# Performance work log

Measured on AMD Instinct MI355X. Metric: run time of the kernel, lower is better.

Reference implementation:

```python
import jax, jax.numpy as jnp
import numpy as np

NUM_CLUSTERS = 8
NUM_ITERS = 3
SIM_TEMP = 10.0
EPS = 1e-12  # F.normalize default eps


def _l2norm(x):
    n = jnp.linalg.norm(x, axis=-1, keepdims=True)
    return x / jnp.maximum(n, EPS)


def setup_inputs() -> dict:
    key = jax.random.key(0)
    ks = jax.random.split(key, 5)
    B, P, C = 8, 16384, 256
    F_p = jax.random.normal(ks[0], (B, P, C), dtype=jnp.float32)
    scale = 1.0 / np.sqrt(C)
    proj_w = jax.random.normal(ks[1], (C, C), dtype=jnp.float32) * scale
    proj_b = jax.random.normal(ks[2], (C,), dtype=jnp.float32) * scale
    refine_w = jax.random.normal(ks[3], (C, C), dtype=jnp.float32) * scale
    refine_b = jax.random.normal(ks[4], (C,), dtype=jnp.float32) * scale
    return {"F_p": F_p, "proj_w": proj_w, "proj_b": proj_b,
            "refine_w": refine_w, "refine_b": refine_b}


def reference(F_p, proj_w, proj_b, refine_w, refine_b):
    B, P, C = F_p.shape
    c = min(NUM_CLUSTERS, P)
    nodes = F_p @ proj_w.T + proj_b  # (B, P, C)
    # initial centers: evenly spaced node indices (torch.linspace(...).long())
    idx = jnp.asarray(np.linspace(0, P - 1, c).astype(np.int64))
    centers = nodes[:, idx, :]  # (B, c, C)
    nodes_norm = _l2norm(nodes)
    for _ in range(NUM_ITERS):
        sim = jnp.einsum('bpc,bkc->bpk', nodes_norm, _l2norm(centers))
        assignments = jnp.argmax(sim, axis=-1)  # (B, P)
        onehot = jax.nn.one_hot(assignments, c, dtype=nodes.dtype)  # (B, P, c)
        counts = jnp.maximum(onehot.sum(axis=1), 1.0)  # (B, c), clamp(min=1)
        # masked mean per cluster == segment mean via one-hot contraction
        centers = jnp.einsum('bpk,bpc->bkc', onehot, nodes) / counts[..., None]
    sim = jnp.einsum('bpc,bkc->bpk', nodes_norm, _l2norm(centers))
    weights = jax.nn.softmax(sim * SIM_TEMP, axis=-1)  # (B, P, c)
    clustered = jnp.einsum('bpk,bkc->bpc', weights, centers)
    return (clustered + F_p) @ refine_w.T + refine_b
```

## Files before the change

kernel.cpp:

```cpp
#include <hip/hip_runtime.h>
#include <hip/hip_bf16.h>
#include <cmath>

#define BB 8
#define PP 16384
#define CC 256
#define NCLUS 8
#define BPROWS (BB*PP)

typedef unsigned int uint;
typedef unsigned short ushort;
typedef __bf16 bf16x8 __attribute__((ext_vector_type(8)));
typedef float f32x16 __attribute__((ext_vector_type(16)));

__device__ __forceinline__ float bflo(uint u){ return __uint_as_float(u << 16); }
__device__ __forceinline__ float bfhi(uint u){ return __uint_as_float(u & 0xffff0000u); }
__device__ __forceinline__ ushort f2bf(float x){ __hip_bfloat16 h = __float2bfloat16(x); return *(ushort*)&h; }
__device__ __forceinline__ uint pk2(float a, float b){ return (uint)f2bf(a) | ((uint)f2bf(b) << 16); }

__global__ __launch_bounds__(256) void wcvt(const float* __restrict__ Wp,
    const float* __restrict__ Wr, ushort* __restrict__ Wpb, ushort* __restrict__ Wrb) {
  int i = blockIdx.x*256 + threadIdx.x;
  float4 a = *(const float4*)(Wp + (size_t)i*4);
  float4 b = *(const float4*)(Wr + (size_t)i*4);
  *(uint2*)(Wpb + (size_t)i*4) = make_uint2(pk2(a.x,a.y), pk2(a.z,a.w));
  *(uint2*)(Wrb + (size_t)i*4) = make_uint2(pk2(b.x,b.y), pk2(b.z,b.w));
}

__global__ __launch_bounds__(256) void fcvt(const float* __restrict__ F, ushort* __restrict__ fb) {
  size_t i = ((size_t)blockIdx.x*256 + threadIdx.x) * 16;
  float4 a = *(const float4*)(F + i);
  float4 b = *(const float4*)(F + i + 4);
  float4 c = *(const float4*)(F + i + 8);
  float4 d = *(const float4*)(F + i + 12);
  *(uint4*)(fb + i)     = make_uint4(pk2(a.x,a.y), pk2(a.z,a.w), pk2(b.x,b.y), pk2(b.z,b.w));
  *(uint4*)(fb + i + 8) = make_uint4(pk2(c.x,c.y), pk2(c.z,c.w), pk2(d.x,d.y), pk2(d.z,d.w));
}

template<bool PROJ>
__global__ __launch_bounds__(512) void gemm_bf16(const ushort* __restrict__ Ab,
    const ushort* __restrict__ Wb, const float* __restrict__ bias,
    void* __restrict__ Dv, float* __restrict__ rnorm,
    const float* __restrict__ W8, const float* __restrict__ CR) {
  __shared__ __align__(16) char AlB[128*64*2];
  __shared__ __align__(16) char WlB[256*64*2];
  __shared__ float rnp[128][4];
  const int t  = threadIdx.x;
  const int p0 = blockIdx.x * 128;
  const int lane = t & 63;
  const int w  = t >> 6;
  const int wr = w >> 2, wc = w & 3;

  const ushort* asrc[2]; char* adst[2];
  #pragma unroll
  for (int i = 0; i < 2; ++i) {
    int S = i*512 + t, row = S >> 3, sc = S & 7;
    asrc[i] = Ab + (size_t)(p0 + row)*CC + ((sc ^ (row & 7)) << 3);
    adst[i] = AlB + (size_t)S*16;
  }
  const ushort* wsrc[4]; char* wdst[4];
  #pragma unroll
  for (int i = 0; i < 4; ++i) {
    int S = i*512 + t, row = S >> 3, sc = S & 7;
    wsrc[i] = Wb + (size_t)row*CC + ((sc ^ (row & 7)) << 3);
    wdst[i] = WlB + (size_t)S*16;
  }
  const int arow = (wr << 6) + (lane & 31);
  const int brow = (wc << 6) + (lane & 31);
  const int kb0  = (lane >> 5) << 4;

  f32x16 acc[2][2];
  #pragma unroll
  for (int fm = 0; fm < 2; ++fm)
    #pragma unroll
    for (int fn = 0; fn < 2; ++fn)
      #pragma unroll
      for (int r = 0; r < 16; ++r) acc[fm][fn][r] = 0.0f;

  #pragma unroll
  for (int ks = 0; ks < 4; ++ks) {
    #pragma unroll
    for (int i = 0; i < 2; ++i)
      __builtin_amdgcn_global_load_lds(
          (const __attribute__((address_space(1))) uint*)(asrc[i] + ks*64),
          (__attribute__((address_space(3))) uint*)adst[i], 16, 0, 0);
    #pragma unroll
    for (int i = 0; i < 4; ++i)
      __builtin_amdgcn_global_load_lds(
          (const __attribute__((address_space(1))) uint*)(wsrc[i] + ks*64),
          (__attribute__((address_space(3))) uint*)wdst[i], 16, 0, 0);
    __syncthreads();
    bf16x8 af[2][4], bg[2][4];
    #pragma unroll
    for (int fm = 0; fm < 2; ++fm)
      #pragma unroll
      for (int kq = 0; kq < 4; ++kq) {
        int row = arow + (fm << 5);
        int off = row*128 + (((kq << 5) + kb0) ^ ((row & 7) << 4));
        af[fm][kq] = *(const bf16x8*)(AlB + off);
      }
    #pragma unroll
    for (int fn = 0; fn < 2; ++fn)
      #pragma unroll
      for (int kq = 0; kq < 4; ++kq) {
        int row = brow + (fn << 5);
        int off = row*128 + (((kq << 5) + kb0) ^ ((row & 7) << 4));
        bg[fn][kq] = *(const bf16x8*)(WlB + off);
      }
    #pragma unroll
    for (int kq = 0; kq < 4; ++kq)
      #pragma unroll
      for (int fm = 0; fm < 2; ++fm)
        #pragma unroll
        for (int fn = 0; fn < 2; ++fn)
          acc[fm][fn] = __builtin_amdgcn_mfma_f32_32x32x16_bf16(
              af[fm][kq], bg[fn][kq], acc[fm][fn], 0, 0, 0);
    if (ks < 3) __syncthreads();
  }

  const int colb = (wc << 6) + (lane & 31);
  const float b0 = bias[colb], b1 = bias[colb + 32];
  float cr0[8], cr1[8];
  if constexpr (!PROJ) {
    const float* crb = CR + (size_t)(blockIdx.x >> 7)*NCLUS*CC;
    #pragma unroll
    for (int k = 0; k < 8; ++k) { cr0[k] = crb[k*CC + colb]; cr1[k] = crb[k*CC + colb + 32]; }
  }
  #pragma unroll
  for (int fm = 0; fm < 2; ++fm) {
    float rs[16];
    #pragma unroll
    for (int r = 0; r < 16; ++r) {
      int rowin = (r & 3) + ((r >> 2) << 3) + ((lane >> 5) << 2);
      size_t grow = (size_t)(p0 + (wr << 6) + (fm << 5) + rowin);
      float v0 = acc[fm][0][r] + b0;
      float v1 = acc[fm][1][r] + b1;
      if constexpr (PROJ) {
        ushort* D = (ushort*)Dv;
        D[grow*CC + colb]      = f2bf(v0);
        D[grow*CC + colb + 32] = f2bf(v1);
        rs[r] = v0*v0 + v1*v1;
      } else {
        float4 ua = *(const float4*)(W8 + grow*8);
        float4 ub = *(const float4*)(W8 + grow*8 + 4);
        v0 += ua.x*cr0[0] + ua.y*cr0[1] + ua.z*cr0[2] + ua.w*cr0[3]
            + ub.x*cr0[4] + ub.y*cr0[5] + ub.z*cr0[6] + ub.w*cr0[7];
        v1 += ua.x*cr1[0] + ua.y*cr1[1] + ua.z*cr1[2] + ua.w*cr1[3]
            + ub.x*cr1[4] + ub.y*cr1[5] + ub.z*cr1[6] + ub.w*cr1[7];
        float* D = (float*)Dv;
        D[grow*CC + colb]      = v0;
        D[grow*CC + colb + 32] = v1;
      }
    }
    if constexpr (PROJ) {
      #pragma unroll
      for (int m = 1; m < 32; m <<= 1)
        #pragma unroll
        for (int r = 0; r < 16; ++r) rs[r] += __shfl_xor(rs[r], m);
      if ((lane & 31) == 0) {
        #pragma unroll
        for (int r = 0; r < 16; ++r) {
          int rowin = (r & 3) + ((r >> 2) << 3) + ((lane >> 5) << 2);
          rnp[(wr << 6) + (fm << 5) + rowin][wc] = rs[r];
        }
      }
    }
  }
  if constexpr (PROJ) {
    __syncthreads();
    if (t < 128) {
      float s = rnp[t][0] + rnp[t][1] + rnp[t][2] + rnp[t][3];
      rnorm[p0 + t] = 1.0f / fmaxf(sqrtf(s), 1e-12f);
    }
  }
}

__global__ void init_centers(const ushort* __restrict__ nbf, float* __restrict__ centers) {
  const int idx[8] = {0, 2340, 4680, 7021, 9361, 11702, 14042, 16383};
  int b = blockIdx.x >> 3, k = blockIdx.x & 7;
  int c = threadIdx.x;
  centers[(size_t)(b*NCLUS + k)*CC + c] =
      __uint_as_float(((uint)nbf[((size_t)b*PP + idx[k])*CC + c]) << 16);
}

__global__ __launch_bounds__(256) void center_norm_init(const float* __restrict__ centers,
    ushort* __restrict__ cnormbf, float* __restrict__ accs, float* __restrict__ counts) {
  const int row = blockIdx.x;
  const int t = threadIdx.x;
  float c = centers[(size_t)row*CC + t];
  float s2 = c*c;
  #pragma unroll
  for (int o = 32; o; o >>= 1) s2 += __shfl_xor(s2, o);
  __shared__ float ps[4];
  if ((t & 63) == 0) ps[t >> 6] = s2;
  __syncthreads();
  float tot = ps[0] + ps[1] + ps[2] + ps[3];
  cnormbf[(size_t)row*CC + t] = f2bf(c * (1.0f / fmaxf(sqrtf(tot), 1e-12f)));
  #pragma unroll
  for (int s = 0; s < 8; ++s) accs[((size_t)s*64 + row)*CC + t] = 0.0f;
  if (t == 0) counts[row] = 0.0f;
}

__global__ __launch_bounds__(256) void centers_finalize(float* __restrict__ accs,
    float* __restrict__ counts, ushort* __restrict__ cnormbf, float* __restrict__ centers) {
  const int row = blockIdx.x;
  const int t = threadIdx.x;
  float v = 0.0f;
  #pragma unroll
  for (int s = 0; s < 8; ++s) {
    v += accs[((size_t)s*64 + row)*CC + t];
    accs[((size_t)s*64 + row)*CC + t] = 0.0f;
  }
  float cnt = fmaxf(counts[row], 1.0f);
  float c = v / cnt;
  centers[(size_t)row*CC + t] = c;
  float s2 = c*c;
  #pragma unroll
  for (int o = 32; o; o >>= 1) s2 += __shfl_xor(s2, o);
  __shared__ float ps[4];
  if ((t & 63) == 0) ps[t >> 6] = s2;
  __syncthreads();
  float tot = ps[0] + ps[1] + ps[2] + ps[3];
  cnormbf[(size_t)row*CC + t] = f2bf(c * (1.0f / fmaxf(sqrtf(tot), 1e-12f)));
  if (t == 0) counts[row] = 0.0f;
}

__global__ __launch_bounds__(256) void cr8_compute(const float* __restrict__ centers,
    const float* __restrict__ Wr, float* __restrict__ CR) {
  __shared__ float cenL[NCLUS][CC];
  const int b = blockIdx.x;
  const int t = threadIdx.x;
  for (int i = t; i < NCLUS*CC; i += 256)
    ((float*)cenL)[i] = centers[(size_t)b*NCLUS*CC + i];
  __syncthreads();
  float a8[8] = {0,0,0,0,0,0,0,0};
  const float* wrow = Wr + (size_t)t*CC;
  for (int j = 0; j < CC; j += 4) {
    float4 wv = *(const float4*)(wrow + j);
    #pragma unroll
    for (int k = 0; k < 8; ++k) {
      float4 cv = *(const float4*)&cenL[k][j];
      a8[k] += cv.x*wv.x + cv.y*wv.y + cv.z*wv.z + cv.w*wv.w;
    }
  }
  #pragma unroll
  for (int k = 0; k < 8; ++k) CR[((size_t)b*NCLUS + k)*CC + t] = a8[k];
}

__device__ __forceinline__ void sims_mfma(const ushort* __restrict__ nb_base,
    const ushort* __restrict__ cnb, int lane, float* s) {
  const int pcol = lane & 31;
  const int kb   = (lane >> 5) << 3;
  const ushort* arow = cnb + (size_t)(pcol & 7)*CC + kb;
  const ushort* brow = nb_base + (size_t)pcol*CC + kb;
  const bool azero = pcol >= 8;
  bf16x8 z;
  #pragma unroll
  for (int j = 0; j < 8; ++j) z[j] = (__bf16)0.0f;
  f32x16 acc;
  #pragma unroll
  for (int r = 0; r < 16; ++r) acc[r] = 0.0f;
  #pragma unroll
  for (int st = 0; st < 16; ++st) {
    bf16x8 af = *(const bf16x8*)(arow + st*16);
    if (azero) af = z;
    bf16x8 bg = *(const bf16x8*)(brow + st*16);
    acc = __builtin_amdgcn_mfma_f32_32x32x16_bf16(af, bg, acc, 0, 0, 0);
  }
  float sh[4];
  #pragma unroll
  for (int r = 0; r < 4; ++r) sh[r] = __shfl_xor(acc[r], 32);
  const bool hi = lane >= 32;
  #pragma unroll
  for (int r = 0; r < 4; ++r) {
    s[r]     = hi ? sh[r]  : acc[r];
    s[r + 4] = hi ? acc[r] : sh[r];
  }
}

__global__ __launch_bounds__(256) void assign_mfma(const ushort* __restrict__ nbf,
    const ushort* __restrict__ cnormbf, float* __restrict__ accs, float* __restrict__ counts) {
  __shared__ int assignL[128];
  __shared__ int cntL[NCLUS];
  const int t = threadIdx.x;
  const int wave = t >> 6, lane = t & 63;
  const int b = blockIdx.x >> 7;
  if (t < NCLUS) cntL[t] = 0;
  __syncthreads();
  const size_t p0w = (size_t)blockIdx.x*128 + wave*32;
  float s[8];
  sims_mfma(nbf + p0w*CC, cnormbf + (size_t)b*NCLUS*CC, lane, s);
  if (lane < 32) {
    int best = 0; float bs = s[0];
    #pragma unroll
    for (int k = 1; k < 8; ++k) if (s[k] > bs) { bs = s[k]; best = k; }
    assignL[wave*32 + lane] = best;
    atomicAdd(&cntL[best], 1);
  }
  __syncthreads();
  float a[8] = {0,0,0,0,0,0,0,0};
  const ushort* base = nbf + (size_t)blockIdx.x*128*CC;
  #pragma unroll 4
  for (int i = 0; i < 128; ++i) {
    int asg = __builtin_amdgcn_readfirstlane(assignL[i]);
    float v = __uint_as_float(((uint)base[(size_t)i*CC + t]) << 16);
    if      (asg == 0) a[0] += v;
    else if (asg == 1) a[1] += v;
    else if (asg == 2) a[2] += v;
    else if (asg == 3) a[3] += v;
    else if (asg == 4) a[4] += v;
    else if (asg == 5) a[5] += v;
    else if (asg == 6) a[6] += v;
    else               a[7] += v;
  }
  const int slot = blockIdx.x & 7;
  float* dst = accs + ((size_t)slot*BB + b)*NCLUS*CC;
  #pragma unroll
  for (int k = 0; k < 8; ++k) atomicAdd(&dst[k*CC + t], a[k]);
  if (t < NCLUS) atomicAdd(&counts[b*NCLUS + t], (float)cntL[t]);
}

__global__ __launch_bounds__(256) void fuse_w8(const ushort* __restrict__ nbf,
    const ushort* __restrict__ cnormbf, const float* __restrict__ rnorm,
    float* __restrict__ W8) {
  const int t = threadIdx.x;
  const int wave = t >> 6, lane = t & 63;
  const int b = blockIdx.x >> 7;
  const size_t p0w = (size_t)blockIdx.x*128 + wave*32;
  float s[8];
  sims_mfma(nbf + p0w*CC, cnormbf + (size_t)b*NCLUS*CC, lane, s);
  const int pcol = lane & 31;
  const float rn10 = rnorm[p0w + pcol] * 10.0f;
  float m = -1e30f;
  #pragma unroll
  for (int k = 0; k < 8; ++k) { s[k] *= rn10; m = fmaxf(m, s[k]); }
  float wgt[8], sw = 0.0f;
  #pragma unroll
  for (int k = 0; k < 8; ++k) { wgt[k] = __expf(s[k] - m); sw += wgt[k]; }
  const float inv = 1.0f / sw;
  if (lane < 32) {
    float* wp = W8 + (p0w + pcol)*8;
    *(float4*)(wp)     = make_float4(wgt[0]*inv, wgt[1]*inv, wgt[2]*inv, wgt[3]*inv);
    *(float4*)(wp + 4) = make_float4(wgt[4]*inv, wgt[5]*inv, wgt[6]*inv, wgt[7]*inv);
  }
}

extern "C" void kernel_launch(void* const* d_in, const int* in_sizes, int n_in,
                              void* d_out, int out_size, void* d_ws, size_t ws_size,
                              hipStream_t stream) {
  const float* F_p      = (const float*)d_in[0];
  const float* proj_w   = (const float*)d_in[1];
  const float* proj_b   = (const float*)d_in[2];
  const float* refine_w = (const float*)d_in[3];
  const float* refine_b = (const float*)d_in[4];
  float* out = (float*)d_out;

  char* ws = (char*)d_ws;
  ushort* nbf    = (ushort*)ws;
  ushort* fbf    = (ushort*)(ws + (size_t)BPROWS*CC*2);
  float*  rnorm  = (float*)(ws + (size_t)BPROWS*CC*4);
  float*  centers= rnorm + BPROWS;
  float*  accs   = centers + BB*NCLUS*CC;
  float*  counts = accs + 8*BB*NCLUS*CC;
  float*  CR     = counts + 64;
  ushort* cnormbf= (ushort*)(CR + BB*NCLUS*CC);
  ushort* Wpb    = cnormbf + BB*NCLUS*CC;
  ushort* Wrb    = Wpb + CC*CC;
  float*  W8     = (float*)(Wrb + CC*CC);

  wcvt<<<64, 256, 0, stream>>>(proj_w, refine_w, Wpb, Wrb);
  fcvt<<<8192, 256, 0, stream>>>(F_p, fbf);
  gemm_bf16<true><<<1024, 512, 0, stream>>>(fbf, Wpb, proj_b, nbf, rnorm, nullptr, nullptr);
  init_centers<<<64, 256, 0, stream>>>(nbf, centers);
  center_norm_init<<<64, 256, 0, stream>>>(centers, cnormbf, accs, counts);
  for (int it = 0; it < 3; ++it) {
    assign_mfma<<<1024, 256, 0, stream>>>(nbf, cnormbf, accs, counts);
    centers_finalize<<<64, 256, 0, stream>>>(accs, counts, cnormbf, centers);
  }
  fuse_w8<<<1024, 256, 0, stream>>>(nbf, cnormbf, rnorm, W8);
  cr8_compute<<<8, 256, 0, stream>>>(centers, refine_w, CR);
  gemm_bf16<false><<<1024, 512, 0, stream>>>(fbf, Wrb, refine_b, out, nullptr, W8, CR);
}
```

Baseline: 303.1 us.

## Fuse fp32-to-bf16 conversion of F_p into projection GEMM A-tile loads

The separate fcvt kernel is removed. The projection GEMM now reads F_p in fp32, packs it to bf16 in registers, writes the tile into swizzled LDS, and also stores the bf16 copy to global memory for reuse by the refine GEMM. This saves one full read pass over F_p and one kernel launch. It adds register prefetching of the next A tile, at the cost of an extra barrier per k-step. Center initialisation is merged into one kernel, and cr8_compute is spread over 64 blocks instead of 8.

```diff
diff --git a/kernel.cpp b/kernel.cpp
--- a/kernel.cpp
+++ b/kernel.cpp
@@ -27,21 +27,12 @@
   *(uint2*)(Wrb + (size_t)i*4) = make_uint2(pk2(b.x,b.y), pk2(b.z,b.w));
 }
 
-__global__ __launch_bounds__(256) void fcvt(const float* __restrict__ F, ushort* __restrict__ fb) {
-  size_t i = ((size_t)blockIdx.x*256 + threadIdx.x) * 16;
-  float4 a = *(const float4*)(F + i);
-  float4 b = *(const float4*)(F + i + 4);
-  float4 c = *(const float4*)(F + i + 8);
-  float4 d = *(const float4*)(F + i + 12);
-  *(uint4*)(fb + i)     = make_uint4(pk2(a.x,a.y), pk2(a.z,a.w), pk2(b.x,b.y), pk2(b.z,b.w));
-  *(uint4*)(fb + i + 8) = make_uint4(pk2(c.x,c.y), pk2(c.z,c.w), pk2(d.x,d.y), pk2(d.z,d.w));
-}
-
 template<bool PROJ>
-__global__ __launch_bounds__(512) void gemm_bf16(const ushort* __restrict__ Ab,
+__global__ __launch_bounds__(512) void gemm_bf16(const void* __restrict__ Av,
     const ushort* __restrict__ Wb, const float* __restrict__ bias,
     void* __restrict__ Dv, float* __restrict__ rnorm,
-    const float* __restrict__ W8, const float* __restrict__ CR) {
+    const float* __restrict__ W8, const float* __restrict__ CR,
+    ushort* __restrict__ fbf) {
   __shared__ __align__(16) char AlB[128*64*2];
   __shared__ __align__(16) char WlB[256*64*2];
   __shared__ float rnp[128][4];
@@ -51,12 +42,18 @@
   const int w  = t >> 6;
   const int wr = w >> 2, wc = w & 3;
 
+  int aoff[2]; size_t agb[2];
   const ushort* asrc[2]; char* adst[2];
   #pragma unroll
   for (int i = 0; i < 2; ++i) {
     int S = i*512 + t, row = S >> 3, sc = S & 7;
-    asrc[i] = Ab + (size_t)(p0 + row)*CC + ((sc ^ (row & 7)) << 3);
-    adst[i] = AlB + (size_t)S*16;
+    if constexpr (PROJ) {
+      aoff[i] = row*128 + ((sc*16) ^ ((row & 7) << 4));
+      agb[i]  = (size_t)(p0 + row)*CC + sc*8;
+    } else {
+      asrc[i] = (const ushort*)Av + (size_t)(p0 + row)*CC + ((sc ^ (row & 7)) << 3);
+      adst[i] = AlB + (size_t)S*16;
+    }
   }
   const ushort* wsrc[4]; char* wdst[4];
   #pragma unroll
@@ -69,27 +66,56 @@
   const int brow = (wc << 6) + (lane & 31);
   const int kb0  = (lane >> 5) << 4;
 
-  f32x16 acc[2][2];
-  #pragma unroll
-  for (int fm = 0; fm < 2; ++fm)
-    #pragma unroll
-    for (int fn = 0; fn < 2; ++fn)
-      #pragma unroll
-      for (int r = 0; r < 16; ++r) acc[fm][fn][r] = 0.0f;
-
-  #pragma unroll
-  for (int ks = 0; ks < 4; ++ks) {
+  uint4 ra[2];
+  auto LOADA = [&](int ks) {
+    const float* A = (const float*)Av;
+    #pragma unroll
+    for (int i = 0; i < 2; ++i) {
+      float4 v0 = *(const float4*)(A + agb[i] + ks*64);
+      float4 v1 = *(const float4*)(A + agb[i] + ks*64 + 4);
+      ra[i] = make_uint4(pk2(v0.x,v0.y), pk2(v0.z,v0.w), pk2(v1.x,v1.y), pk2(v1.z,v1.w));
+    }
+  };
+  auto WRITEA = [&](int ks) {
+    #pragma unroll
+    for (int i = 0; i < 2; ++i) {
+      *(uint4*)(AlB + aoff[i]) = ra[i];
+      *(uint4*)(fbf + agb[i] + ks*64) = ra[i];
+    }
+  };
+  auto STAGEA_LDS = [&](int ks) {
     #pragma unroll
     for (int i = 0; i < 2; ++i)
       __builtin_amdgcn_global_load_lds(
           (const __attribute__((address_space(1))) uint*)(asrc[i] + ks*64),
           (__attribute__((address_space(3))) uint*)adst[i], 16, 0, 0);
+  };
+  auto STAGEW = [&](int ks) {
     #pragma unroll
     for (int i = 0; i < 4; ++i)
       __builtin_amdgcn_global_load_lds(
           (const __attribute__((address_space(1))) uint*)(wsrc[i] + ks*64),
           (__attribute__((address_space(3))) uint*)wdst[i], 16, 0, 0);
-    __syncthreads();
+  };
+
+  f32x16 acc[2][2];
+  #pragma unroll
+  for (int fm = 0; fm < 2; ++fm)
+    #pragma unroll
+    for (int fn = 0; fn < 2; ++fn)
+      #pragma unroll
+      for (int r = 0; r < 16; ++r) acc[fm][fn][r] = 0.0f;
+
+  if constexpr (PROJ) {
+    LOADA(0); STAGEW(0); WRITEA(0);
+  } else {
+    STAGEA_LDS(0); STAGEW(0);
+  }
+  __syncthreads();
+
+  #pragma unroll
+  for (int ks = 0; ks < 4; ++ks) {
+    if constexpr (PROJ) { if (ks < 3) LOADA(ks+1); }
     bf16x8 af[2][4], bg[2][4];
     #pragma unroll
     for (int fm = 0; fm < 2; ++fm)
@@ -115,7 +141,12 @@
         for (int fn = 0; fn < 2; ++fn)
           acc[fm][fn] = __builtin_amdgcn_mfma_f32_32x32x16_bf16(
               af[fm][kq], bg[fn][kq], acc[fm][fn], 0, 0, 0);
-    if (ks < 3) __syncthreads();
+    if (ks < 3) {
+      __syncthreads();
+      if constexpr (PROJ) { STAGEW(ks+1); WRITEA(ks+1); }
+      else               { STAGEA_LDS(ks+1); STAGEW(ks+1); }
+      __syncthreads();
+    }
   }
 
   const int colb = (wc << 6) + (lane & 31);
@@ -175,19 +206,15 @@
   }
 }
 
-__global__ void init_centers(const ushort* __restrict__ nbf, float* __restrict__ centers) {
-  const int idx[8] = {0, 2340, 4680, 7021, 9361, 11702, 14042, 16383};
-  int b = blockIdx.x >> 3, k = blockIdx.x & 7;
-  int c = threadIdx.x;
-  centers[(size_t)(b*NCLUS + k)*CC + c] =
-      __uint_as_float(((uint)nbf[((size_t)b*PP + idx[k])*CC + c]) << 16);
-}
-
-__global__ __launch_bounds__(256) void center_norm_init(const float* __restrict__ centers,
-    ushort* __restrict__ cnormbf, float* __restrict__ accs, float* __restrict__ counts) {
+__global__ __launch_bounds__(256) void centers_init(const ushort* __restrict__ nbf,
+    float* __restrict__ centers, ushort* __restrict__ cnormbf,
+    float* __restrict__ accs, float* __restrict__ counts) {
+  const int idxs[8] = {0, 2340, 4680, 7021, 9361, 11702, 14042, 16383};
   const int row = blockIdx.x;
+  const int b = row >> 3, k = row & 7;
   const int t = threadIdx.x;
-  float c = centers[(size_t)row*CC + t];
+  float c = __uint_as_float(((uint)nbf[((size_t)b*PP + idxs[k])*CC + t]) << 16);
+  centers[(size_t)row*CC + t] = c;
   float s2 = c*c;
   #pragma unroll
   for (int o = 32; o; o >>= 1) s2 += __shfl_xor(s2, o);
@@ -227,24 +254,20 @@
 
 __global__ __launch_bounds__(256) void cr8_compute(const float* __restrict__ centers,
     const float* __restrict__ Wr, float* __restrict__ CR) {
-  __shared__ float cenL[NCLUS][CC];
-  const int b = blockIdx.x;
+  __shared__ float cenL[CC];
+  const int row = blockIdx.x;
   const int t = threadIdx.x;
-  for (int i = t; i < NCLUS*CC; i += 256)
-    ((float*)cenL)[i] = centers[(size_t)b*NCLUS*CC + i];
-  __syncthreads();
-  float a8[8] = {0,0,0,0,0,0,0,0};
+  cenL[t] = centers[(size_t)row*CC + t];
+  __syncthreads();
+  float a = 0.0f;
   const float* wrow = Wr + (size_t)t*CC;
+  #pragma unroll 4
   for (int j = 0; j < CC; j += 4) {
     float4 wv = *(const float4*)(wrow + j);
-    #pragma unroll
-    for (int k = 0; k < 8; ++k) {
-      float4 cv = *(const float4*)&cenL[k][j];
-      a8[k] += cv.x*wv.x + cv.y*wv.y + cv.z*wv.z + cv.w*wv.w;
-    }
-  }
-  #pragma unroll
-  for (int k = 0; k < 8; ++k) CR[((size_t)b*NCLUS + k)*CC + t] = a8[k];
+    float4 cv = *(const float4*)&cenL[j];
+    a += cv.x*wv.x + cv.y*wv.y + cv.z*wv.z + cv.w*wv.w;
+  }
+  CR[(size_t)row*CC + t] = a;
 }
 
 __device__ __forceinline__ void sims_mfma(const ushort* __restrict__ nb_base,
@@ -369,15 +392,13 @@
   float*  W8     = (float*)(Wrb + CC*CC);
 
   wcvt<<<64, 256, 0, stream>>>(proj_w, refine_w, Wpb, Wrb);
-  fcvt<<<8192, 256, 0, stream>>>(F_p, fbf);
-  gemm_bf16<true><<<1024, 512, 0, stream>>>(fbf, Wpb, proj_b, nbf, rnorm, nullptr, nullptr);
-  init_centers<<<64, 256, 0, stream>>>(nbf, centers);
-  center_norm_init<<<64, 256, 0, stream>>>(centers, cnormbf, accs, counts);
+  gemm_bf16<true><<<1024, 512, 0, stream>>>(F_p, Wpb, proj_b, nbf, rnorm, nullptr, nullptr, fbf);
+  centers_init<<<64, 256, 0, stream>>>(nbf, centers, cnormbf, accs, counts);
   for (int it = 0; it < 3; ++it) {
     assign_mfma<<<1024, 256, 0, stream>>>(nbf, cnormbf, accs, counts);
     centers_finalize<<<64, 256, 0, stream>>>(accs, counts, cnormbf, centers);
   }
   fuse_w8<<<1024, 256, 0, stream>>>(nbf, cnormbf, rnorm, W8);
-  cr8_compute<<<8, 256, 0, stream>>>(centers, refine_w, CR);
-  gemm_bf16<false><<<1024, 512, 0, stream>>>(fbf, Wrb, refine_b, out, nullptr, W8, CR);
-}
+  cr8_compute<<<64, 256, 0, stream>>>(centers, refine_w, CR);
+  gemm_bf16<false><<<1024, 512, 0, stream>>>(fbf, Wrb, refine_b, out, nullptr, W8, CR, nullptr);
+}
```

Measured after the change: 285.0 us. -6.0%, faster.
